# Kernel optimization log

Hardware: AMD Instinct MI355X
Metric: run time of the kernel (lower is better)

## Reference

```python
import jax, jax.numpy as jnp
import numpy as np

N_NODES = 100000
N_EDGES = 3200000
IN_CH = 256
OUT_CH = 1


def setup_inputs() -> dict:
    key = jax.random.key(0)
    ks = jax.random.split(key, 8)
    x = jax.random.normal(ks[0], (N_NODES, IN_CH), dtype=jnp.float32)
    edge_index = jax.random.randint(ks[1], (2, N_EDGES), 0, N_NODES, dtype=jnp.int64 if jax.config.jax_enable_x64 else jnp.int32)
    s_in = 1.0 / np.sqrt(IN_CH)
    Wq = jax.random.uniform(ks[2], (IN_CH, OUT_CH), jnp.float32, -s_in, s_in)
    bq = jax.random.uniform(ks[3], (OUT_CH,), jnp.float32, -s_in, s_in)
    Wk = jax.random.uniform(ks[4], (IN_CH, OUT_CH), jnp.float32, -s_in, s_in)
    bk = jax.random.uniform(ks[5], (OUT_CH,), jnp.float32, -s_in, s_in)
    Wv = jax.random.uniform(ks[6], (IN_CH, IN_CH), jnp.float32, -s_in, s_in)
    bv = jax.random.uniform(ks[7], (IN_CH,), jnp.float32, -s_in, s_in)
    return {"x": x, "edge_index": edge_index, "Wq": Wq, "bq": bq,
            "Wk": Wk, "bk": bk, "Wv": Wv, "bv": bv}


def reference(x, edge_index, Wq, bq, Wk, bk, Wv, bv):
    num_nodes = x.shape[0]
    q = x @ Wq + bq                       # [N, out_ch]
    k = x @ Wk + bk                       # [N, out_ch]
    v = x @ Wv + bv                       # [N, in_ch]
    row, col = edge_index[0], edge_index[1]
    # edge attention logits: gather + dot over out_ch
    att = jnp.sum(q[row] * k[col], axis=-1)          # [E]
    att = jax.nn.leaky_relu(att, negative_slope=0.2)
    att = jax.nn.softmax(att, axis=0)                # softmax over ALL edges (dim=0)
    # scatter-add edge attention to source nodes
    attention_weights = jax.ops.segment_sum(att, row, num_segments=num_nodes)  # [N]
    graph_emb = jnp.sum(attention_weights[:, None] * v, axis=0)                # [in_ch]
    return graph_emb, attention_weights
```

## Files before the change

### kernel.cpp

```cpp
#include <hip/hip_runtime.h>

#define N_NODES 100000
#define N_EDGES 3200000
#define CH 256

#define EPB_S 4096
#define GS 782
#define NB2 25
#define BSZ 4096
#define G_AGG 10
#define SLICE 79
#define GRID_QK 1563
#define GRID_POOL 512
#define YCOPY 16

#define OFF_M      0
#define OFF_TOTAL  1
#define OFF_QKMM   16
#define OFF_PTOT   6272
#define OFF_YU16   6672
#define OFF_PRE    10768
#define OFF_Q      31104
#define OFF_K      131104
#define OFF_AWU    231104
#define OFF_PART   331104
#define OFF_EX     1355104
#define OFF_ROW    4558176

__global__ __launch_bounds__(256) void k_init(float* p, int cnt) {
    int i = blockIdx.x * 256 + threadIdx.x;
    if (i < cnt) p[i] = 0.0f;
}

__global__ __launch_bounds__(256) void k_qk(const float* __restrict__ x,
                                            const float* __restrict__ Wq,
                                            const float* __restrict__ bq,
                                            const float* __restrict__ Wk,
                                            const float* __restrict__ bk,
                                            float* __restrict__ q,
                                            float* __restrict__ k,
                                            float4* __restrict__ qkmm) {
    int w = threadIdx.x >> 6, lane = threadIdx.x & 63;
    float4 wq = ((const float4*)Wq)[lane];
    float4 wk = ((const float4*)Wk)[lane];
    float bqs = bq[0], bks = bk[0];
    float qmax = -3.0e38f, qmin = 3.0e38f, kmax = -3.0e38f, kmin = 3.0e38f;
    int base = blockIdx.x * 64 + w * 16;
    #pragma unroll 4
    for (int i = 0; i < 16; ++i) {
        int n = base + i;
        if (n < N_NODES) {
            float4 xv = ((const float4*)(x + (size_t)n * CH))[lane];
            float dq = fmaf(xv.x, wq.x, fmaf(xv.y, wq.y, fmaf(xv.z, wq.z, xv.w * wq.w)));
            float dk = fmaf(xv.x, wk.x, fmaf(xv.y, wk.y, fmaf(xv.z, wk.z, xv.w * wk.w)));
            #pragma unroll
            for (int off = 32; off; off >>= 1) {
                dq += __shfl_down(dq, off);
                dk += __shfl_down(dk, off);
            }
            if (lane == 0) {
                float qq = dq + bqs, kk = dk + bks;
                q[n] = qq; k[n] = kk;
                qmax = fmaxf(qmax, qq); qmin = fminf(qmin, qq);
                kmax = fmaxf(kmax, kk); kmin = fminf(kmin, kk);
            }
        }
    }
    __shared__ float4 sm[4];
    if (lane == 0) sm[w] = make_float4(qmax, qmin, kmax, kmin);
    __syncthreads();
    if (threadIdx.x == 0) {
        float4 r = sm[0];
        #pragma unroll
        for (int j = 1; j < 4; ++j) {
            r.x = fmaxf(r.x, sm[j].x); r.y = fminf(r.y, sm[j].y);
            r.z = fmaxf(r.z, sm[j].z); r.w = fminf(r.w, sm[j].w);
        }
        qkmm[blockIdx.x] = r;
    }
}

__global__ __launch_bounds__(256) void k_bound(const float4* __restrict__ qkmm,
                                               float* __restrict__ mp) {
    int t = threadIdx.x;
    float qmax = -3.0e38f, qmin = 3.0e38f, kmax = -3.0e38f, kmin = 3.0e38f;
    for (int i = t; i < GRID_QK; i += 256) {
        float4 r = qkmm[i];
        qmax = fmaxf(qmax, r.x); qmin = fminf(qmin, r.y);
        kmax = fmaxf(kmax, r.z); kmin = fminf(kmin, r.w);
    }
    #pragma unroll
    for (int off = 32; off; off >>= 1) {
        qmax = fmaxf(qmax, __shfl_down(qmax, off));
        qmin = fminf(qmin, __shfl_down(qmin, off));
        kmax = fmaxf(kmax, __shfl_down(kmax, off));
        kmin = fminf(kmin, __shfl_down(kmin, off));
    }
    __shared__ float4 smf[4];
    if ((t & 63) == 0) smf[t >> 6] = make_float4(qmax, qmin, kmax, kmin);
    __syncthreads();
    if (t == 0) {
        float4 r = smf[0];
        #pragma unroll
        for (int j = 1; j < 4; ++j) {
            r.x = fmaxf(r.x, smf[j].x); r.y = fminf(r.y, smf[j].y);
            r.z = fmaxf(r.z, smf[j].z); r.w = fminf(r.w, smf[j].w);
        }
        float p = fmaxf(fmaxf(r.x * r.z, r.x * r.w), fmaxf(r.y * r.z, r.y * r.w));
        mp[0] = (p >= 0.0f) ? p : 0.2f * p;
    }
}

__global__ __launch_bounds__(256) void k_sort(const int* __restrict__ ei,
                                              const float* __restrict__ q,
                                              const float* __restrict__ k,
                                              const float* __restrict__ mp,
                                              float* __restrict__ ex_out,
                                              unsigned short* __restrict__ row_out,
                                              int* __restrict__ pre) {
    __shared__ int cnt[NB2];
    __shared__ int pos[NB2];
    __shared__ int pref[NB2 + 1];
    __shared__ float lex[EPB_S];
    __shared__ unsigned short lrow[EPB_S];
    int t = threadIdx.x, blk = blockIdx.x;
    int e0 = blk * EPB_S;
    int ecnt = min(EPB_S, N_EDGES - e0);
    for (int i = t; i < NB2; i += 256) cnt[i] = 0;
    float m = mp[0];
    __syncthreads();

    int rr[16]; float ee[16];
    #pragma unroll
    for (int j = 0; j < 16; ++j) {
        int i = j * 256 + t;
        if (i < ecnt) {
            int r = ei[e0 + i], c = ei[N_EDGES + e0 + i];
            float v = q[r] * k[c];
            v = (v >= 0.0f) ? v : 0.2f * v;
            rr[j] = r;
            ee[j] = __expf(v - m);
            atomicAdd(&cnt[r >> 12], 1);
        }
    }
    __syncthreads();
    if (t == 0) {
        int run = 0;
        #pragma unroll
        for (int b = 0; b < NB2; ++b) { pref[b] = run; pos[b] = run; run += cnt[b]; }
        pref[NB2] = run;
    }
    __syncthreads();
    if (t < NB2 + 1) pre[blk * 26 + t] = pref[t];
    #pragma unroll
    for (int j = 0; j < 16; ++j) {
        int i = j * 256 + t;
        if (i < ecnt) {
            int b = rr[j] >> 12;
            int p = atomicAdd(&pos[b], 1);
            lex[p] = ee[j];
            lrow[p] = (unsigned short)(rr[j] & (BSZ - 1));
        }
    }
    __syncthreads();
    size_t base = (size_t)blk * EPB_S;
    for (int i = t; i < ecnt; i += 256) ex_out[base + i] = lex[i];
    unsigned* ro = (unsigned*)(row_out + base);
    const unsigned* lr = (const unsigned*)lrow;
    int words = (ecnt + 1) >> 1;
    for (int i = t; i < words; i += 256) ro[i] = lr[i];
}

__global__ __launch_bounds__(256) void k_agg(const float* __restrict__ ex,
                                             const unsigned short* __restrict__ row,
                                             const int* __restrict__ pre,
                                             float* __restrict__ partial) {
    int b = blockIdx.x / G_AGG, g = blockIdx.x % G_AGG;
    __shared__ float acc[BSZ];
    __shared__ int seg[SLICE][2];
    int t = threadIdx.x;
    for (int i = t; i < BSZ; i += 256) acc[i] = 0.0f;
    int blk0 = g * SLICE, blk1 = min(blk0 + SLICE, GS);
    int nseg = blk1 - blk0;
    for (int i = t; i < nseg; i += 256) {
        seg[i][0] = pre[(blk0 + i) * 26 + b];
        seg[i][1] = pre[(blk0 + i) * 26 + b + 1];
    }
    __syncthreads();
    for (int sI = 0; sI < nseg; ++sI) {
        size_t base = (size_t)(blk0 + sI) * EPB_S;
        int s0 = seg[sI][0], s1 = seg[sI][1];
        for (int i = s0 + t; i < s1; i += 256)
            atomicAdd(&acc[row[base + i]], ex[base + i]);
    }
    __syncthreads();
    float* dst = partial + ((size_t)b * G_AGG + g) * BSZ;
    for (int i = t; i < BSZ; i += 256) dst[i] = acc[i];
}

__global__ __launch_bounds__(256) void k_fold(const float* __restrict__ partial,
                                              float* __restrict__ awu,
                                              float* __restrict__ ptot) {
    int t = threadIdx.x;
    int n = blockIdx.x * 256 + t;
    float s = 0.0f;
    if (n < N_NODES) {
        int b = n >> 12, off = n & (BSZ - 1);
        const float* p = partial + (size_t)b * G_AGG * BSZ + off;
        #pragma unroll
        for (int g = 0; g < G_AGG; ++g) s += p[(size_t)g * BSZ];
        awu[n] = s;
    }
    float r = s;
    #pragma unroll
    for (int off = 32; off; off >>= 1) r += __shfl_down(r, off);
    __shared__ float sm[4];
    if ((t & 63) == 0) sm[t >> 6] = r;
    __syncthreads();
    if (t == 0) ptot[blockIdx.x] = sm[0] + sm[1] + sm[2] + sm[3];
}

__global__ __launch_bounds__(256) void k_total2(const float* __restrict__ ptot,
                                                int n, float* __restrict__ totalp) {
    int t = threadIdx.x;
    float s = 0.0f;
    for (int i = t; i < n; i += 256) s += ptot[i];
    #pragma unroll
    for (int off = 32; off; off >>= 1) s += __shfl_down(s, off);
    __shared__ float sm[4];
    if ((t & 63) == 0) sm[t >> 6] = s;
    __syncthreads();
    if (t == 0) totalp[0] = sm[0] + sm[1] + sm[2] + sm[3];
}

__global__ __launch_bounds__(256) void k_pool(const float* __restrict__ x,
                                              const float* __restrict__ awu,
                                              const float* __restrict__ totalp,
                                              float* __restrict__ yu16,
                                              float* __restrict__ aw_out) {
    int t = threadIdx.x, s = t >> 6, g = t & 63;
    const float4* X4 = (const float4*)x;
    float4 acc = make_float4(0.f, 0.f, 0.f, 0.f);
    for (int base = blockIdx.x * 8; base < N_NODES; base += GRID_POOL * 8) {
        float a0 = awu[base + s];
        float a1 = awu[base + 4 + s];
        float4 x0 = X4[(size_t)(base + s) * 64 + g];
        float4 x1 = X4[(size_t)(base + 4 + s) * 64 + g];
        acc.x = fmaf(a0, x0.x, acc.x); acc.y = fmaf(a0, x0.y, acc.y);
        acc.z = fmaf(a0, x0.z, acc.z); acc.w = fmaf(a0, x0.w, acc.w);
        acc.x = fmaf(a1, x1.x, acc.x); acc.y = fmaf(a1, x1.y, acc.y);
        acc.z = fmaf(a1, x1.z, acc.z); acc.w = fmaf(a1, x1.w, acc.w);
    }
    __shared__ float4 tmp4[4][64];
    tmp4[s][g] = acc;
    __syncthreads();
    const float* tmp = (const float*)tmp4;
    int c = t;
    float sum = tmp[0 * 256 + c] + tmp[1 * 256 + c] + tmp[2 * 256 + c] + tmp[3 * 256 + c];
    atomicAdd(&yu16[(blockIdx.x & (YCOPY - 1)) * 256 + c], sum);
    float inv = 1.0f / totalp[0];
    for (int i = blockIdx.x * 256 + t; i < N_NODES; i += GRID_POOL * 256)
        aw_out[i] = awu[i] * inv;
}

__global__ __launch_bounds__(256) void k_final(const float* __restrict__ yu16,
                                               const float* __restrict__ totalp,
                                               const float* __restrict__ Wv,
                                               const float* __restrict__ bv,
                                               float* __restrict__ out) {
    int t = threadIdx.x, b = blockIdx.x;
    float inv = 1.0f / totalp[0];
    float y = 0.0f;
    #pragma unroll
    for (int j = 0; j < YCOPY; ++j) y += yu16[j * 256 + t];
    y *= inv;
    float val = y * Wv[(size_t)t * CH + b];
    #pragma unroll
    for (int off = 32; off; off >>= 1) val += __shfl_down(val, off);
    __shared__ float sm[4];
    if ((t & 63) == 0) sm[t >> 6] = val;
    __syncthreads();
    if (t == 0) out[b] = sm[0] + sm[1] + sm[2] + sm[3] + bv[b];
}

extern "C" void kernel_launch(void* const* d_in, const int* in_sizes, int n_in,
                              void* d_out, int out_size, void* d_ws, size_t ws_size,
                              hipStream_t stream) {
    const float* x  = (const float*)d_in[0];
    const int*   ei = (const int*)d_in[1];
    const float* Wq = (const float*)d_in[2];
    const float* bq = (const float*)d_in[3];
    const float* Wk = (const float*)d_in[4];
    const float* bk = (const float*)d_in[5];
    const float* Wv = (const float*)d_in[6];
    const float* bv = (const float*)d_in[7];
    float* out = (float*)d_out;
    float* ws  = (float*)d_ws;

    float*          mp      = ws + OFF_M;
    float*          totalp  = ws + OFF_TOTAL;
    float4*         qkmm    = (float4*)(ws + OFF_QKMM);
    float*          ptot    = ws + OFF_PTOT;
    float*          yu16    = ws + OFF_YU16;
    int*            pre     = (int*)(ws + OFF_PRE);
    float*          q       = ws + OFF_Q;
    float*          k       = ws + OFF_K;
    float*          awu     = ws + OFF_AWU;
    float*          partial = ws + OFF_PART;
    float*          ex      = ws + OFF_EX;
    unsigned short* row     = (unsigned short*)(ws + OFF_ROW);

    hipLaunchKernelGGL(k_init, dim3(16), dim3(256), 0, stream, yu16, 4096);
    hipLaunchKernelGGL(k_qk, dim3(GRID_QK), dim3(256), 0, stream,
                       x, Wq, bq, Wk, bk, q, k, qkmm);
    hipLaunchKernelGGL(k_bound, dim3(1), dim3(256), 0, stream, qkmm, mp);
    hipLaunchKernelGGL(k_sort, dim3(GS), dim3(256), 0, stream,
                       ei, q, k, mp, ex, row, pre);
    hipLaunchKernelGGL(k_agg, dim3(NB2 * G_AGG), dim3(256), 0, stream,
                       ex, row, pre, partial);
    hipLaunchKernelGGL(k_fold, dim3((N_NODES + 255) / 256), dim3(256), 0, stream,
                       partial, awu, ptot);
    hipLaunchKernelGGL(k_total2, dim3(1), dim3(256), 0, stream,
                       ptot, (N_NODES + 255) / 256, totalp);
    hipLaunchKernelGGL(k_pool, dim3(GRID_POOL), dim3(256), 0, stream,
                       x, awu, totalp, yu16, out + CH);
    hipLaunchKernelGGL(k_final, dim3(CH), dim3(256), 0, stream,
                       yu16, totalp, Wv, bv, out);
}
```

Baseline: 297.0 us.

## Drop softmax max bound, fuse small kernels, widen sort/agg blocks, retile final GEMV

Removes the q/k min-max pass and its bound kernel, so edge logits are exponentiated without subtracting a maximum. This avoids a kernel launch and a reduction but can overflow for large logits. The yu16 zeroing moves into k_qk, and the total-sum reduction moves into k_pool, which removes two more tiny launches. The sort runs 512 threads over 8192 edges per block with per-wave bucket counters to reduce shared-atomic contention, and aggregation gives each wave its own segment. k_qk processes four nodes per wave with 16-lane reductions, and k_final computes 32 output columns per block.

```diff
diff --git a/kernel.cpp b/kernel.cpp
--- a/kernel.cpp
+++ b/kernel.cpp
@@ -4,33 +4,26 @@
 #define N_EDGES 3200000
 #define CH 256
 
-#define EPB_S 4096
-#define GS 782
+#define EPB_S 8192
+#define GS 391
 #define NB2 25
 #define BSZ 4096
 #define G_AGG 10
-#define SLICE 79
+#define SLICE 40
 #define GRID_QK 1563
 #define GRID_POOL 512
 #define YCOPY 16
 
-#define OFF_M      0
-#define OFF_TOTAL  1
-#define OFF_QKMM   16
-#define OFF_PTOT   6272
-#define OFF_YU16   6672
-#define OFF_PRE    10768
-#define OFF_Q      31104
-#define OFF_K      131104
-#define OFF_AWU    231104
-#define OFF_PART   331104
-#define OFF_EX     1355104
-#define OFF_ROW    4558176
-
-__global__ __launch_bounds__(256) void k_init(float* p, int cnt) {
-    int i = blockIdx.x * 256 + threadIdx.x;
-    if (i < cnt) p[i] = 0.0f;
-}
+#define OFF_TOTAL  0
+#define OFF_PTOT   16
+#define OFF_YU16   528
+#define OFF_PRE    4624
+#define OFF_Q      14800
+#define OFF_K      114800
+#define OFF_AWU    214800
+#define OFF_PART   314800
+#define OFF_EX     1338800
+#define OFF_ROW    4541872
 
 __global__ __launch_bounds__(256) void k_qk(const float* __restrict__ x,
                                             const float* __restrict__ Wq,
@@ -39,163 +32,129 @@
                                             const float* __restrict__ bk,
                                             float* __restrict__ q,
                                             float* __restrict__ k,
-                                            float4* __restrict__ qkmm) {
-    int w = threadIdx.x >> 6, lane = threadIdx.x & 63;
-    float4 wq = ((const float4*)Wq)[lane];
-    float4 wk = ((const float4*)Wk)[lane];
+                                            float* __restrict__ yu16) {
+    int t = threadIdx.x;
+    if (blockIdx.x < 16) yu16[blockIdx.x * 256 + t] = 0.0f;
+    int w = t >> 6, lane = t & 63;
+    int g = lane >> 4, seg = lane & 15;
+    float4 wq4[4], wk4[4];
+    #pragma unroll
+    for (int j = 0; j < 4; ++j) {
+        wq4[j] = ((const float4*)Wq)[seg + 16 * j];
+        wk4[j] = ((const float4*)Wk)[seg + 16 * j];
+    }
     float bqs = bq[0], bks = bk[0];
-    float qmax = -3.0e38f, qmin = 3.0e38f, kmax = -3.0e38f, kmin = 3.0e38f;
-    int base = blockIdx.x * 64 + w * 16;
-    #pragma unroll 4
-    for (int i = 0; i < 16; ++i) {
-        int n = base + i;
+    int base = blockIdx.x * 64 + w * 16 + g;
+    #pragma unroll
+    for (int i = 0; i < 4; ++i) {
+        int n = base + i * 4;
         if (n < N_NODES) {
-            float4 xv = ((const float4*)(x + (size_t)n * CH))[lane];
-            float dq = fmaf(xv.x, wq.x, fmaf(xv.y, wq.y, fmaf(xv.z, wq.z, xv.w * wq.w)));
-            float dk = fmaf(xv.x, wk.x, fmaf(xv.y, wk.y, fmaf(xv.z, wk.z, xv.w * wk.w)));
+            const float4* xr = (const float4*)(x + (size_t)n * CH);
+            float dq = 0.0f, dk = 0.0f;
             #pragma unroll
-            for (int off = 32; off; off >>= 1) {
-                dq += __shfl_down(dq, off);
-                dk += __shfl_down(dk, off);
+            for (int j = 0; j < 4; ++j) {
+                float4 xv = xr[seg + 16 * j];
+                dq = fmaf(xv.x, wq4[j].x, fmaf(xv.y, wq4[j].y,
+                     fmaf(xv.z, wq4[j].z, fmaf(xv.w, wq4[j].w, dq))));
+                dk = fmaf(xv.x, wk4[j].x, fmaf(xv.y, wk4[j].y,
+                     fmaf(xv.z, wk4[j].z, fmaf(xv.w, wk4[j].w, dk))));
             }
-            if (lane == 0) {
-                float qq = dq + bqs, kk = dk + bks;
-                q[n] = qq; k[n] = kk;
-                qmax = fmaxf(qmax, qq); qmin = fminf(qmin, qq);
-                kmax = fmaxf(kmax, kk); kmin = fminf(kmin, kk);
-            }
+            dq += __shfl_down(dq, 8); dq += __shfl_down(dq, 4);
+            dq += __shfl_down(dq, 2); dq += __shfl_down(dq, 1);
+            dk += __shfl_down(dk, 8); dk += __shfl_down(dk, 4);
+            dk += __shfl_down(dk, 2); dk += __shfl_down(dk, 1);
+            if (seg == 0) { q[n] = dq + bqs; k[n] = dk + bks; }
         }
     }
-    __shared__ float4 sm[4];
-    if (lane == 0) sm[w] = make_float4(qmax, qmin, kmax, kmin);
-    __syncthreads();
-    if (threadIdx.x == 0) {
-        float4 r = sm[0];
-        #pragma unroll
-        for (int j = 1; j < 4; ++j) {
-            r.x = fmaxf(r.x, sm[j].x); r.y = fminf(r.y, sm[j].y);
-            r.z = fmaxf(r.z, sm[j].z); r.w = fminf(r.w, sm[j].w);
-        }
-        qkmm[blockIdx.x] = r;
-    }
-}
-
-__global__ __launch_bounds__(256) void k_bound(const float4* __restrict__ qkmm,
-                                               float* __restrict__ mp) {
-    int t = threadIdx.x;
-    float qmax = -3.0e38f, qmin = 3.0e38f, kmax = -3.0e38f, kmin = 3.0e38f;
-    for (int i = t; i < GRID_QK; i += 256) {
-        float4 r = qkmm[i];
-        qmax = fmaxf(qmax, r.x); qmin = fminf(qmin, r.y);
-        kmax = fmaxf(kmax, r.z); kmin = fminf(kmin, r.w);
-    }
-    #pragma unroll
-    for (int off = 32; off; off >>= 1) {
-        qmax = fmaxf(qmax, __shfl_down(qmax, off));
-        qmin = fminf(qmin, __shfl_down(qmin, off));
-        kmax = fmaxf(kmax, __shfl_down(kmax, off));
-        kmin = fminf(kmin, __shfl_down(kmin, off));
-    }
-    __shared__ float4 smf[4];
-    if ((t & 63) == 0) smf[t >> 6] = make_float4(qmax, qmin, kmax, kmin);
-    __syncthreads();
-    if (t == 0) {
-        float4 r = smf[0];
-        #pragma unroll
-        for (int j = 1; j < 4; ++j) {
-            r.x = fmaxf(r.x, smf[j].x); r.y = fminf(r.y, smf[j].y);
-            r.z = fmaxf(r.z, smf[j].z); r.w = fminf(r.w, smf[j].w);
-        }
-        float p = fmaxf(fmaxf(r.x * r.z, r.x * r.w), fmaxf(r.y * r.z, r.y * r.w));
-        mp[0] = (p >= 0.0f) ? p : 0.2f * p;
-    }
-}
-
-__global__ __launch_bounds__(256) void k_sort(const int* __restrict__ ei,
+}
+
+__global__ __launch_bounds__(512) void k_sort(const int* __restrict__ ei,
                                               const float* __restrict__ q,
                                               const float* __restrict__ k,
-                                              const float* __restrict__ mp,
                                               float* __restrict__ ex_out,
                                               unsigned short* __restrict__ row_out,
                                               int* __restrict__ pre) {
-    __shared__ int cnt[NB2];
-    __shared__ int pos[NB2];
+    __shared__ int cnt[8][NB2];
+    __shared__ int base8[8][NB2];
     __shared__ int pref[NB2 + 1];
+    __shared__ int bsum[NB2];
     __shared__ float lex[EPB_S];
     __shared__ unsigned short lrow[EPB_S];
-    int t = threadIdx.x, blk = blockIdx.x;
+    int t = threadIdx.x, blk = blockIdx.x, w = t >> 6;
     int e0 = blk * EPB_S;
     int ecnt = min(EPB_S, N_EDGES - e0);
-    for (int i = t; i < NB2; i += 256) cnt[i] = 0;
-    float m = mp[0];
-    __syncthreads();
-
+    for (int i = t; i < 8 * NB2; i += 512) ((int*)cnt)[i] = 0;
+    __syncthreads();
     int rr[16]; float ee[16];
     #pragma unroll
     for (int j = 0; j < 16; ++j) {
-        int i = j * 256 + t;
+        int i = j * 512 + t;
         if (i < ecnt) {
             int r = ei[e0 + i], c = ei[N_EDGES + e0 + i];
             float v = q[r] * k[c];
             v = (v >= 0.0f) ? v : 0.2f * v;
-            rr[j] = r;
-            ee[j] = __expf(v - m);
-            atomicAdd(&cnt[r >> 12], 1);
-        }
+            rr[j] = r; ee[j] = __expf(v);
+            atomicAdd(&cnt[w][r >> 12], 1);
+        } else rr[j] = -1;
+    }
+    __syncthreads();
+    if (t < NB2) {
+        int s = 0;
+        #pragma unroll
+        for (int ww = 0; ww < 8; ++ww) { base8[ww][t] = s; s += cnt[ww][t]; }
+        bsum[t] = s;
     }
     __syncthreads();
     if (t == 0) {
         int run = 0;
         #pragma unroll
-        for (int b = 0; b < NB2; ++b) { pref[b] = run; pos[b] = run; run += cnt[b]; }
+        for (int b = 0; b < NB2; ++b) { pref[b] = run; run += bsum[b]; }
         pref[NB2] = run;
     }
     __syncthreads();
+    if (t < 8 * NB2) {
+        int ww = t / NB2, b = t - ww * NB2;
+        base8[ww][b] += pref[b];
+    }
     if (t < NB2 + 1) pre[blk * 26 + t] = pref[t];
+    __syncthreads();
     #pragma unroll
     for (int j = 0; j < 16; ++j) {
-        int i = j * 256 + t;
-        if (i < ecnt) {
+        if (rr[j] >= 0) {
             int b = rr[j] >> 12;
-            int p = atomicAdd(&pos[b], 1);
+            int p = atomicAdd(&base8[w][b], 1);
             lex[p] = ee[j];
             lrow[p] = (unsigned short)(rr[j] & (BSZ - 1));
         }
     }
     __syncthreads();
-    size_t base = (size_t)blk * EPB_S;
-    for (int i = t; i < ecnt; i += 256) ex_out[base + i] = lex[i];
-    unsigned* ro = (unsigned*)(row_out + base);
+    size_t gb = (size_t)blk * EPB_S;
+    for (int i = t; i < ecnt; i += 512) ex_out[gb + i] = lex[i];
+    unsigned* ro = (unsigned*)(row_out + gb);
     const unsigned* lr = (const unsigned*)lrow;
     int words = (ecnt + 1) >> 1;
-    for (int i = t; i < words; i += 256) ro[i] = lr[i];
-}
-
-__global__ __launch_bounds__(256) void k_agg(const float* __restrict__ ex,
+    for (int i = t; i < words; i += 512) ro[i] = lr[i];
+}
+
+__global__ __launch_bounds__(512) void k_agg(const float* __restrict__ ex,
                                              const unsigned short* __restrict__ row,
                                              const int* __restrict__ pre,
                                              float* __restrict__ partial) {
     int b = blockIdx.x / G_AGG, g = blockIdx.x % G_AGG;
     __shared__ float acc[BSZ];
-    __shared__ int seg[SLICE][2];
-    int t = threadIdx.x;
-    for (int i = t; i < BSZ; i += 256) acc[i] = 0.0f;
-    int blk0 = g * SLICE, blk1 = min(blk0 + SLICE, GS);
-    int nseg = blk1 - blk0;
-    for (int i = t; i < nseg; i += 256) {
-        seg[i][0] = pre[(blk0 + i) * 26 + b];
-        seg[i][1] = pre[(blk0 + i) * 26 + b + 1];
-    }
-    __syncthreads();
-    for (int sI = 0; sI < nseg; ++sI) {
-        size_t base = (size_t)(blk0 + sI) * EPB_S;
-        int s0 = seg[sI][0], s1 = seg[sI][1];
-        for (int i = s0 + t; i < s1; i += 256)
-            atomicAdd(&acc[row[base + i]], ex[base + i]);
+    int t = threadIdx.x, w = t >> 6, lane = t & 63;
+    for (int i = t; i < BSZ; i += 512) acc[i] = 0.0f;
+    __syncthreads();
+    int sb0 = g * SLICE, sb1 = min(sb0 + SLICE, GS);
+    for (int sb = sb0 + w; sb < sb1; sb += 8) {
+        size_t gbase = (size_t)sb * EPB_S;
+        int s0 = pre[sb * 26 + b], s1 = pre[sb * 26 + b + 1];
+        for (int i = s0 + lane; i < s1; i += 64)
+            atomicAdd(&acc[row[gbase + i]], ex[gbase + i]);
     }
     __syncthreads();
     float* dst = partial + ((size_t)b * G_AGG + g) * BSZ;
-    for (int i = t; i < BSZ; i += 256) dst[i] = acc[i];
+    for (int i = t; i < BSZ; i += 512) dst[i] = acc[i];
 }
 
 __global__ __launch_bounds__(256) void k_fold(const float* __restrict__ partial,
@@ -220,25 +179,27 @@
     if (t == 0) ptot[blockIdx.x] = sm[0] + sm[1] + sm[2] + sm[3];
 }
 
-__global__ __launch_bounds__(256) void k_total2(const float* __restrict__ ptot,
-                                                int n, float* __restrict__ totalp) {
-    int t = threadIdx.x;
-    float s = 0.0f;
-    for (int i = t; i < n; i += 256) s += ptot[i];
-    #pragma unroll
-    for (int off = 32; off; off >>= 1) s += __shfl_down(s, off);
-    __shared__ float sm[4];
-    if ((t & 63) == 0) sm[t >> 6] = s;
-    __syncthreads();
-    if (t == 0) totalp[0] = sm[0] + sm[1] + sm[2] + sm[3];
-}
-
 __global__ __launch_bounds__(256) void k_pool(const float* __restrict__ x,
                                               const float* __restrict__ awu,
-                                              const float* __restrict__ totalp,
+                                              const float* __restrict__ ptot,
+                                              float* __restrict__ totalp,
                                               float* __restrict__ yu16,
                                               float* __restrict__ aw_out) {
     int t = threadIdx.x, s = t >> 6, g = t & 63;
+    float ts = ptot[t] + ((t + 256 < GS) ? ptot[t + 256] : 0.0f);
+    #pragma unroll
+    for (int off = 32; off; off >>= 1) ts += __shfl_down(ts, off);
+    __shared__ float sm[4];
+    __shared__ float tot;
+    if (g == 0) sm[s] = ts;
+    __syncthreads();
+    if (t == 0) {
+        tot = sm[0] + sm[1] + sm[2] + sm[3];
+        if (blockIdx.x == 0) totalp[0] = tot;
+    }
+    __syncthreads();
+    float inv = 1.0f / tot;
+
     const float4* X4 = (const float4*)x;
     float4 acc = make_float4(0.f, 0.f, 0.f, 0.f);
     for (int base = blockIdx.x * 8; base < N_NODES; base += GRID_POOL * 8) {
@@ -255,10 +216,8 @@
     tmp4[s][g] = acc;
     __syncthreads();
     const float* tmp = (const float*)tmp4;
-    int c = t;
-    float sum = tmp[0 * 256 + c] + tmp[1 * 256 + c] + tmp[2 * 256 + c] + tmp[3 * 256 + c];
-    atomicAdd(&yu16[(blockIdx.x & (YCOPY - 1)) * 256 + c], sum);
-    float inv = 1.0f / totalp[0];
+    float sum = tmp[0 * 256 + t] + tmp[1 * 256 + t] + tmp[2 * 256 + t] + tmp[3 * 256 + t];
+    atomicAdd(&yu16[(blockIdx.x & (YCOPY - 1)) * 256 + t], sum);
     for (int i = blockIdx.x * 256 + t; i < N_NODES; i += GRID_POOL * 256)
         aw_out[i] = awu[i] * inv;
 }
@@ -268,19 +227,30 @@
                                                const float* __restrict__ Wv,
                                                const float* __restrict__ bv,
                                                float* __restrict__ out) {
-    int t = threadIdx.x, b = blockIdx.x;
+    __shared__ float ysh[256];
+    __shared__ float red[256];
+    int t = threadIdx.x;
     float inv = 1.0f / totalp[0];
-    float y = 0.0f;
-    #pragma unroll
-    for (int j = 0; j < YCOPY; ++j) y += yu16[j * 256 + t];
-    y *= inv;
-    float val = y * Wv[(size_t)t * CH + b];
-    #pragma unroll
-    for (int off = 32; off; off >>= 1) val += __shfl_down(val, off);
-    __shared__ float sm[4];
-    if ((t & 63) == 0) sm[t >> 6] = val;
-    __syncthreads();
-    if (t == 0) out[b] = sm[0] + sm[1] + sm[2] + sm[3] + bv[b];
+    float yv = 0.0f;
+    #pragma unroll
+    for (int j = 0; j < YCOPY; ++j) yv += yu16[j * 256 + t];
+    ysh[t] = yv * inv;
+    __syncthreads();
+    int c = blockIdx.x * 32 + (t & 31), rg = t >> 5;
+    float acc = 0.0f;
+    #pragma unroll
+    for (int j = 0; j < 32; ++j) {
+        int kk = rg * 32 + j;
+        acc = fmaf(ysh[kk], Wv[(size_t)kk * CH + c], acc);
+    }
+    red[t] = acc;
+    __syncthreads();
+    if (t < 32) {
+        float sv = 0.0f;
+        #pragma unroll
+        for (int j = 0; j < 8; ++j) sv += red[j * 32 + t];
+        out[blockIdx.x * 32 + t] = sv + bv[blockIdx.x * 32 + t];
+    }
 }
 
 extern "C" void kernel_launch(void* const* d_in, const int* in_sizes, int n_in,
@@ -297,9 +267,7 @@
     float* out = (float*)d_out;
     float* ws  = (float*)d_ws;
 
-    float*          mp      = ws + OFF_M;
     float*          totalp  = ws + OFF_TOTAL;
-    float4*         qkmm    = (float4*)(ws + OFF_QKMM);
     float*          ptot    = ws + OFF_PTOT;
     float*          yu16    = ws + OFF_YU16;
     int*            pre     = (int*)(ws + OFF_PRE);
@@ -310,20 +278,16 @@
     float*          ex      = ws + OFF_EX;
     unsigned short* row     = (unsigned short*)(ws + OFF_ROW);
 
-    hipLaunchKernelGGL(k_init, dim3(16), dim3(256), 0, stream, yu16, 4096);
     hipLaunchKernelGGL(k_qk, dim3(GRID_QK), dim3(256), 0, stream,
-                       x, Wq, bq, Wk, bk, q, k, qkmm);
-    hipLaunchKernelGGL(k_bound, dim3(1), dim3(256), 0, stream, qkmm, mp);
-    hipLaunchKernelGGL(k_sort, dim3(GS), dim3(256), 0, stream,
-                       ei, q, k, mp, ex, row, pre);
-    hipLaunchKernelGGL(k_agg, dim3(NB2 * G_AGG), dim3(256), 0, stream,
+                       x, Wq, bq, Wk, bk, q, k, yu16);
+    hipLaunchKernelGGL(k_sort, dim3(GS), dim3(512), 0, stream,
+                       ei, q, k, ex, row, pre);
+    hipLaunchKernelGGL(k_agg, dim3(NB2 * G_AGG), dim3(512), 0, stream,
                        ex, row, pre, partial);
     hipLaunchKernelGGL(k_fold, dim3((N_NODES + 255) / 256), dim3(256), 0, stream,
                        partial, awu, ptot);
-    hipLaunchKernelGGL(k_total2, dim3(1), dim3(256), 0, stream,
-                       ptot, (N_NODES + 255) / 256, totalp);
     hipLaunchKernelGGL(k_pool, dim3(GRID_POOL), dim3(256), 0, stream,
-                       x, awu, totalp, yu16, out + CH);
-    hipLaunchKernelGGL(k_final, dim3(CH), dim3(256), 0, stream,
+                       x, awu, ptot, totalp, yu16, out + CH);
+    hipLaunchKernelGGL(k_final, dim3(8), dim3(256), 0, stream,
                        yu16, totalp, Wv, bv, out);
 }
```

Measured after the change: 269.6 us. 1.1x faster.
